# Kernel optimization log

Hardware: AMD Instinct MI355X
Metric: run time of the kernel (lower is better)

Reference implementation:

```python
import jax, jax.numpy as jnp
import numpy as np

B, SQ, SK, D = 8, 4096, 4096, 64


def setup_inputs() -> dict:
    key = jax.random.key(0)
    k1, k2, k3 = jax.random.split(key, 3)
    x1 = jax.random.normal(k1, (B, SQ, D), dtype=jnp.float32)   # queries
    x2 = jax.random.normal(k2, (B, SK, D), dtype=jnp.float32)   # keys
    x3 = jax.random.normal(k3, (B, SK, D), dtype=jnp.float32)   # values
    x4 = 0                                                      # dropout p (static, 0 => deterministic)
    x5 = jnp.ones((1,), dtype=jnp.float32)                      # scale divisor
    return {"x1": x1, "x2": x2, "x3": x3, "x4": x4, "x5": x5}


def reference(x1, x2, x3, x4, x5):
    # scores: [B, Sq, Sk]
    scores = jnp.einsum("bqd,bkd->bqk", x1, x2) / x5
    attn = jax.nn.softmax(scores, axis=-1)
    p = float(x4)  # static python scalar
    if p > 0.0:
        mask = jax.random.bernoulli(jax.random.key(42), 1.0 - p, attn.shape)
        attn = attn * mask.astype(attn.dtype) / (1.0 - p)
    # out: [B, Sq, D]
    return jnp.einsum("bqk,bkd->bqd", attn, x3)
```

## Files before the change

kernel.cpp:

```cpp
#include <hip/hip_runtime.h>


typedef _Float16 f16x8 __attribute__((ext_vector_type(8)));
typedef _Float16 f16x4 __attribute__((ext_vector_type(4)));
typedef __fp16   h16x2 __attribute__((ext_vector_type(2)));
typedef float    f32x4 __attribute__((ext_vector_type(4)));

constexpr int kB  = 8;
constexpr int kSQ = 4096;
constexpr int kSK = 4096;
constexpr int kD  = 64;
constexpr int KSPLIT = 4;
constexpr int SKH = kSK / KSPLIT;
constexpr int BQ  = 256;
constexpr int MT  = 4;
constexpr int BK  = 64;
constexpr size_t APART = (size_t)kB * kSQ * kD;
constexpr float kLog2e = 1.44269504088896340736f;

static __device__ __forceinline__ f16x4 pack4(float a, float b, float c, float d) {
    h16x2 p0 = __builtin_amdgcn_cvt_pkrtz(a, b);
    h16x2 p1 = __builtin_amdgcn_cvt_pkrtz(c, d);
    f16x4 r;
    r[0] = (_Float16)p0[0]; r[1] = (_Float16)p0[1];
    r[2] = (_Float16)p1[0]; r[3] = (_Float16)p1[1];
    return r;
}
static __device__ __forceinline__ f16x8 pack8(const float4& a, const float4& c) {
    f16x4 lo = pack4(a.x, a.y, a.z, a.w);
    f16x4 hi = pack4(c.x, c.y, c.z, c.w);
    f16x8 f;
    f[0] = lo[0]; f[1] = lo[1]; f[2] = lo[2]; f[3] = lo[3];
    f[4] = hi[0]; f[5] = hi[1]; f[6] = hi[2]; f[7] = hi[3];
    return f;
}

typedef const __attribute__((address_space(1))) unsigned int* gu32p;
typedef __attribute__((address_space(3))) unsigned int* lu32p;
static __device__ __forceinline__ void gload_lds16(const void* g, void* l) {
    __builtin_amdgcn_global_load_lds((gu32p)g, (lu32p)l, 16, 0, 0);
}

__global__ __launch_bounds__(256, 2)
void fattn_prepass(const float* __restrict__ Kg,
                   const float* __restrict__ Vg,
                   _Float16* __restrict__ Kh,
                   _Float16* __restrict__ Vt)
{
    __shared__ _Float16 tr[kD][BK];

    const int tid = threadIdx.x;
    const int kt  = blockIdx.x;
    const int b   = blockIdx.y;

    const int k = tid >> 2;
    const int p = tid & 3;
    const int gk = kt * BK + k;

    {
        const float* src = Kg + ((size_t)b * kSK + gk) * kD + p * 16;
        const float4 a0 = *(const float4*)(src + 0);
        const float4 a1 = *(const float4*)(src + 4);
        const float4 a2 = *(const float4*)(src + 8);
        const float4 a3 = *(const float4*)(src + 12);
        _Float16* dst = Kh + ((size_t)b * kSK + gk) * kD;
        const int fb0 = 2 * p, fb1 = 2 * p + 1;
        *(f16x8*)&dst[(fb0 ^ (gk & 7)) * 8] = pack8(a0, a1);
        *(f16x8*)&dst[(fb1 ^ (gk & 7)) * 8] = pack8(a2, a3);
    }
    {
        const float* src = Vg + ((size_t)b * kSK + gk) * kD + p * 16;
        const float4 a0 = *(const float4*)(src + 0);
        const float4 a1 = *(const float4*)(src + 4);
        const float4 a2 = *(const float4*)(src + 8);
        const float4 a3 = *(const float4*)(src + 12);
        const float v[16] = {a0.x,a0.y,a0.z,a0.w, a1.x,a1.y,a1.z,a1.w,
                             a2.x,a2.y,a2.z,a2.w, a3.x,a3.y,a3.z,a3.w};
#pragma unroll
        for (int j = 0; j < 16; ++j)
            tr[p * 16 + j][k] = (_Float16)v[j];
    }
    __syncthreads();
    {
        const int f  = tid >> 2;
        const int p2 = tid & 3;
        const f16x8 b0 = *(const f16x8*)&tr[f][p2 * 16 + 0];
        const f16x8 b1 = *(const f16x8*)&tr[f][p2 * 16 + 8];
        _Float16* dst = Vt + (((size_t)b * 64 + kt) * kD + f) * BK;
        const int kb0 = 2 * p2, kb1 = 2 * p2 + 1;
        *(f16x8*)&dst[(kb0 ^ (f & 7)) * 8] = b0;
        *(f16x8*)&dst[(kb1 ^ (f & 7)) * 8] = b1;
    }
}

__global__ __launch_bounds__(256, 2)
void fattn_partial(const float* __restrict__ Qg,
                   const _Float16* __restrict__ Kh,
                   const _Float16* __restrict__ Vt,
                   const float* __restrict__ sdiv,
                   _Float16* __restrict__ Ap,
                   float2* __restrict__ MLp)
{
    __shared__ __align__(16) _Float16 sK[2][BK * kD];
    __shared__ __align__(16) _Float16 sV[2][kD * BK];
    __shared__ __align__(16) _Float16 sP[4][16][BK];

    const int tid  = threadIdx.x;
    const int w    = tid >> 6;
    const int lane = tid & 63;
    const int l16  = lane & 15;
    const int quad = lane >> 4;
    const int sw   = (quad ^ (l16 & 7)) * 8;
    const int swp  = (l16 & 7) * 8;

    const int flat = blockIdx.x;
    const int c    = flat & 31;
    const int qi   = flat >> 5;
    const int b    = c >> 2;
    const int ks   = c & 3;
    const int qb   = qi * BQ;

    const float qscale = kLog2e / sdiv[0];

    const float* Qb = Qg + ((size_t)b * kSQ + qb) * kD;
    const _Float16* Khb = Kh + ((size_t)b * kSK + (size_t)ks * SKH) * kD;
    const _Float16* Vtb = Vt + (((size_t)b * 64 + (size_t)ks * (SKH / BK)) * kD) * BK;

    f16x8 qf[MT][2];
#pragma unroll
    for (int mt = 0; mt < MT; ++mt) {
        const float* qrow = Qb + (size_t)(w * 64 + mt * 16 + l16) * kD;
#pragma unroll
        for (int kk = 0; kk < 2; ++kk) {
            const float4 a = *(const float4*)(qrow + kk * 32 + quad * 8);
            const float4 cc = *(const float4*)(qrow + kk * 32 + quad * 8 + 4);
            float4 as = make_float4(a.x * qscale, a.y * qscale, a.z * qscale, a.w * qscale);
            float4 cs = make_float4(cc.x * qscale, cc.y * qscale, cc.z * qscale, cc.w * qscale);
            qf[mt][kk] = pack8(as, cs);
        }
    }

    f16x8 ones;
#pragma unroll
    for (int j = 0; j < 8; ++j) ones[j] = (_Float16)1.0f;

    auto stage = [&](int kt, int buf) {
        const char* gk = (const char*)(Khb + (size_t)kt * BK * kD) + w * 2048 + lane * 16;
        const char* gv = (const char*)(Vtb + (size_t)kt * kD * BK) + w * 2048 + lane * 16;
        char* lk = (char*)&sK[buf][0] + w * 2048;
        char* lv = (char*)&sV[buf][0] + w * 2048;
        gload_lds16(gk,        lk);
        gload_lds16(gk + 1024, lk + 1024);
        gload_lds16(gv,        lv);
        gload_lds16(gv + 1024, lv + 1024);
    };

    f32x4 o[MT][4];
    f32x4 ol[MT];
    float m_i[MT];
#pragma unroll
    for (int mt = 0; mt < MT; ++mt) {
        m_i[mt] = -1e30f;
#pragma unroll
        for (int r = 0; r < 4; ++r) ol[mt][r] = 0.0f;
#pragma unroll
        for (int dt = 0; dt < 4; ++dt)
#pragma unroll
            for (int r = 0; r < 4; ++r) o[mt][dt][r] = 0.0f;
    }

    stage(0, 0);
    __syncthreads();

    const int nIter = SKH / BK;
    for (int kt = 0; kt < nIter; ++kt) {
        const int buf = kt & 1;
        const bool more = (kt + 1 < nIter);
        if (more) stage(kt + 1, buf ^ 1);

        f32x4 s[MT][4];
#pragma unroll
        for (int nt = 0; nt < 4; ++nt) {
            const int krow = (nt * 16 + l16) * kD;
            const f16x8 kf0 = *(const f16x8*)&sK[buf][krow + sw];
            const f16x8 kf1 = *(const f16x8*)&sK[buf][krow + (sw ^ 32)];
#pragma unroll
            for (int mt = 0; mt < MT; ++mt) {
                f32x4 acc;
#pragma unroll
                for (int r = 0; r < 4; ++r) acc[r] = 0.0f;
                acc = __builtin_amdgcn_mfma_f32_16x16x32_f16(kf0, qf[mt][0], acc, 0, 0, 0);
                acc = __builtin_amdgcn_mfma_f32_16x16x32_f16(kf1, qf[mt][1], acc, 0, 0, 0);
                s[mt][nt] = acc;
            }
        }

        f16x8 vf[4][2];
#pragma unroll
        for (int dt = 0; dt < 4; ++dt) {
            const int frow = (dt * 16 + l16) * BK;
            vf[dt][0] = *(const f16x8*)&sV[buf][frow + sw];
            vf[dt][1] = *(const f16x8*)&sV[buf][frow + (sw ^ 32)];
        }

#pragma unroll
        for (int mt = 0; mt < MT; ++mt) {
            float ra = fmaxf(fmaxf(s[mt][0][0], s[mt][0][1]), fmaxf(s[mt][0][2], s[mt][0][3]));
            float rb = fmaxf(fmaxf(s[mt][1][0], s[mt][1][1]), fmaxf(s[mt][1][2], s[mt][1][3]));
            float rc = fmaxf(fmaxf(s[mt][2][0], s[mt][2][1]), fmaxf(s[mt][2][2], s[mt][2][3]));
            float rd = fmaxf(fmaxf(s[mt][3][0], s[mt][3][1]), fmaxf(s[mt][3][2], s[mt][3][3]));
            float rm = fmaxf(fmaxf(ra, rb), fmaxf(rc, rd));
            rm = fmaxf(rm, __shfl_xor(rm, 16, 64));
            rm = fmaxf(rm, __shfl_xor(rm, 32, 64));
            const float mnew = fmaxf(m_i[mt], rm);
#pragma unroll
            for (int nt = 0; nt < 4; ++nt)
#pragma unroll
                for (int r = 0; r < 4; ++r)
                    s[mt][nt][r] = __builtin_amdgcn_exp2f(s[mt][nt][r] - mnew);
            if (!__all(mnew == m_i[mt])) {
                const float alpha = __builtin_amdgcn_exp2f(m_i[mt] - mnew);
                ol[mt][0] *= alpha;
#pragma unroll
                for (int dt = 0; dt < 4; ++dt)
#pragma unroll
                    for (int r = 0; r < 4; ++r) o[mt][dt][r] *= alpha;
            }
            m_i[mt] = mnew;

#pragma unroll
            for (int nt = 0; nt < 4; ++nt)
                *(f16x4*)&sP[w][l16][(nt * 16 + quad * 4) ^ swp] =
                    pack4(s[mt][nt][0], s[mt][nt][1], s[mt][nt][2], s[mt][nt][3]);

            const f16x8 pf0 = *(const f16x8*)&sP[w][l16][(quad * 8) ^ swp];
            const f16x8 pf1 = *(const f16x8*)&sP[w][l16][(32 + quad * 8) ^ swp];
#pragma unroll
            for (int dt = 0; dt < 4; ++dt) {
                o[mt][dt] = __builtin_amdgcn_mfma_f32_16x16x32_f16(vf[dt][0], pf0, o[mt][dt], 0, 0, 0);
                o[mt][dt] = __builtin_amdgcn_mfma_f32_16x16x32_f16(vf[dt][1], pf1, o[mt][dt], 0, 0, 0);
            }
            ol[mt] = __builtin_amdgcn_mfma_f32_16x16x32_f16(ones, pf0, ol[mt], 0, 0, 0);
            ol[mt] = __builtin_amdgcn_mfma_f32_16x16x32_f16(ones, pf1, ol[mt], 0, 0, 0);
        }

        __syncthreads();
    }

    _Float16* Ab = Ap + (size_t)ks * APART + ((size_t)b * kSQ + qb) * kD;
    float2* MLb = MLp + (size_t)ks * kB * kSQ + (size_t)b * kSQ + qb;
#pragma unroll
    for (int mt = 0; mt < MT; ++mt) {
        const int row = w * 64 + mt * 16 + l16;
#pragma unroll
        for (int dt = 0; dt < 4; ++dt)
            *(f16x4*)&Ab[(size_t)row * kD + dt * 16 + quad * 4] =
                pack4(o[mt][dt][0], o[mt][dt][1], o[mt][dt][2], o[mt][dt][3]);
        if (quad == 0) MLb[row] = make_float2(m_i[mt], ol[mt][0]);
    }
}

__global__ __launch_bounds__(256)
void fattn_combine(const _Float16* __restrict__ Ap,
                   const float2* __restrict__ MLp,
                   float* __restrict__ Og)
{
    const int idx = blockIdx.x * 256 + threadIdx.x;
    const int r = idx >> 4;
    const int c = (idx & 15) * 4;

    float m = -1e30f;
    float2 ml[KSPLIT];
#pragma unroll
    for (int s = 0; s < KSPLIT; ++s) {
        ml[s] = MLp[(size_t)s * kB * kSQ + r];
        m = fmaxf(m, ml[s].x);
    }
    float acc[4] = {0.f, 0.f, 0.f, 0.f};
    float lsum = 0.f;
#pragma unroll
    for (int s = 0; s < KSPLIT; ++s) {
        const float e = __builtin_amdgcn_exp2f(ml[s].x - m);
        lsum += e * ml[s].y;
        const f16x4 a = *(const f16x4*)&Ap[(size_t)s * APART + (size_t)r * kD + c];
#pragma unroll
        for (int j = 0; j < 4; ++j) acc[j] += e * (float)a[j];
    }
    const float inv = 1.0f / lsum;
    float4 res = make_float4(acc[0] * inv, acc[1] * inv, acc[2] * inv, acc[3] * inv);
    *(float4*)&Og[(size_t)r * kD + c] = res;
}

extern "C" void kernel_launch(void* const* d_in, const int* in_sizes, int n_in,
                              void* d_out, int out_size, void* d_ws, size_t ws_size,
                              hipStream_t stream) {
    const float* Q    = (const float*)d_in[0];
    const float* K    = (const float*)d_in[1];
    const float* V    = (const float*)d_in[2];
    const float* sdiv = (const float*)d_in[4];
    float* O = (float*)d_out;

    _Float16* Kh  = (_Float16*)d_ws;
    _Float16* Vt  = Kh + (size_t)kB * kSK * kD;
    _Float16* Ap  = Vt + (size_t)kB * kSK * kD;
    float2*   MLp = (float2*)(Ap + (size_t)KSPLIT * APART);

    fattn_prepass<<<dim3(kSK / BK, kB), dim3(256), 0, stream>>>(K, V, Kh, Vt);
    fattn_partial<<<dim3((kSQ / BQ) * kB * KSPLIT), dim3(256), 0, stream>>>(Q, Kh, Vt, sdiv, Ap, MLp);
    fattn_combine<<<dim3(kB * kSQ * kD / (256 * 4)), dim3(256), 0, stream>>>(Ap, MLp, O);
}
```

Measured before the change: 138.8 us.

## Switch attention partial kernel to 32x32x16 MFMA with register-resident P via permlane swap

Rewrites the partial attention kernel to use 32x32x16 MFMA tiles with one 32-row query tile per wave and BQ reduced to 128. The P matrix is repacked in registers with permlane32_swap instead of going through LDS, and the row sum is accumulated with scalar adds instead of a ones-MFMA. Launch bounds are raised to allow 4 blocks per CU. The aim is to cut LDS traffic and per-tile MFMA overhead and to raise occupancy. In exchange, each block does less work on the K/V tiles it loads, so global and LDS staging per query grows.

```diff
diff --git a/kernel.cpp b/kernel.cpp
--- a/kernel.cpp
+++ b/kernel.cpp
@@ -5,6 +5,7 @@
 typedef _Float16 f16x4 __attribute__((ext_vector_type(4)));
 typedef __fp16   h16x2 __attribute__((ext_vector_type(2)));
 typedef float    f32x4 __attribute__((ext_vector_type(4)));
+typedef float    f32x16 __attribute__((ext_vector_type(16)));
 
 constexpr int kB  = 8;
 constexpr int kSQ = 4096;
@@ -12,8 +13,7 @@
 constexpr int kD  = 64;
 constexpr int KSPLIT = 4;
 constexpr int SKH = kSK / KSPLIT;
-constexpr int BQ  = 256;
-constexpr int MT  = 4;
+constexpr int BQ  = 128;
 constexpr int BK  = 64;
 constexpr size_t APART = (size_t)kB * kSQ * kD;
 constexpr float kLog2e = 1.44269504088896340736f;
@@ -34,12 +34,29 @@
     f[4] = hi[0]; f[5] = hi[1]; f[6] = hi[2]; f[7] = hi[3];
     return f;
 }
+static __device__ __forceinline__ unsigned pkrtz_u(float a, float b) {
+    union { h16x2 h; unsigned u; } cv;
+    cv.h = __builtin_amdgcn_cvt_pkrtz(a, b);
+    return cv.u;
+}
 
 typedef const __attribute__((address_space(1))) unsigned int* gu32p;
 typedef __attribute__((address_space(3))) unsigned int* lu32p;
 static __device__ __forceinline__ void gload_lds16(const void* g, void* l) {
     __builtin_amdgcn_global_load_lds((gu32p)g, (lu32p)l, 16, 0, 0);
 }
+
+#define PA_SLICE(dst, sv, rb) do {                                          \
+    unsigned c0 = pkrtz_u((sv)[(rb)+0], (sv)[(rb)+1]);                      \
+    unsigned c1 = pkrtz_u((sv)[(rb)+2], (sv)[(rb)+3]);                      \
+    unsigned c2 = pkrtz_u((sv)[(rb)+4], (sv)[(rb)+5]);                      \
+    unsigned c3 = pkrtz_u((sv)[(rb)+6], (sv)[(rb)+7]);                      \
+    auto r02 = __builtin_amdgcn_permlane32_swap(c0, c2, false, false);      \
+    auto r13 = __builtin_amdgcn_permlane32_swap(c1, c3, false, false);      \
+    union { unsigned u[4]; f16x8 v; } _r;                                   \
+    _r.u[0] = r02[0]; _r.u[1] = r13[0]; _r.u[2] = r02[1]; _r.u[3] = r13[1]; \
+    dst = _r.v;                                                             \
+} while (0)
 
 __global__ __launch_bounds__(256, 2)
 void fattn_prepass(const float* __restrict__ Kg,
@@ -93,7 +110,7 @@
     }
 }
 
-__global__ __launch_bounds__(256, 2)
+__global__ __launch_bounds__(256, 4)
 void fattn_partial(const float* __restrict__ Qg,
                    const _Float16* __restrict__ Kh,
                    const _Float16* __restrict__ Vt,
@@ -103,15 +120,12 @@
 {
     __shared__ __align__(16) _Float16 sK[2][BK * kD];
     __shared__ __align__(16) _Float16 sV[2][kD * BK];
-    __shared__ __align__(16) _Float16 sP[4][16][BK];
 
     const int tid  = threadIdx.x;
     const int w    = tid >> 6;
     const int lane = tid & 63;
-    const int l16  = lane & 15;
-    const int quad = lane >> 4;
-    const int sw   = (quad ^ (l16 & 7)) * 8;
-    const int swp  = (l16 & 7) * 8;
+    const int l31  = lane & 31;
+    const int hi   = lane >> 5;
 
     const int flat = blockIdx.x;
     const int c    = flat & 31;
@@ -126,23 +140,23 @@
     const _Float16* Khb = Kh + ((size_t)b * kSK + (size_t)ks * SKH) * kD;
     const _Float16* Vtb = Vt + (((size_t)b * 64 + (size_t)ks * (SKH / BK)) * kD) * BK;
 
-    f16x8 qf[MT][2];
-#pragma unroll
-    for (int mt = 0; mt < MT; ++mt) {
-        const float* qrow = Qb + (size_t)(w * 64 + mt * 16 + l16) * kD;
-#pragma unroll
-        for (int kk = 0; kk < 2; ++kk) {
-            const float4 a = *(const float4*)(qrow + kk * 32 + quad * 8);
-            const float4 cc = *(const float4*)(qrow + kk * 32 + quad * 8 + 4);
+    f16x8 qf[4];
+    {
+        const float* qrow = Qb + (size_t)(w * 32 + l31) * kD;
+#pragma unroll
+        for (int ds = 0; ds < 4; ++ds) {
+            const float4 a  = *(const float4*)(qrow + ds * 16 + hi * 8);
+            const float4 cc = *(const float4*)(qrow + ds * 16 + hi * 8 + 4);
             float4 as = make_float4(a.x * qscale, a.y * qscale, a.z * qscale, a.w * qscale);
             float4 cs = make_float4(cc.x * qscale, cc.y * qscale, cc.z * qscale, cc.w * qscale);
-            qf[mt][kk] = pack8(as, cs);
-        }
-    }
-
-    f16x8 ones;
-#pragma unroll
-    for (int j = 0; j < 8; ++j) ones[j] = (_Float16)1.0f;
+            qf[ds] = pack8(as, cs);
+        }
+    }
+
+    int offA[4];
+#pragma unroll
+    for (int i = 0; i < 4; ++i)
+        offA[i] = l31 * 64 + (((2 * i + hi) ^ (l31 & 7)) * 8);
 
     auto stage = [&](int kt, int buf) {
         const char* gk = (const char*)(Khb + (size_t)kt * BK * kD) + w * 2048 + lane * 16;
@@ -155,19 +169,11 @@
         gload_lds16(gv + 1024, lv + 1024);
     };
 
-    f32x4 o[MT][4];
-    f32x4 ol[MT];
-    float m_i[MT];
-#pragma unroll
-    for (int mt = 0; mt < MT; ++mt) {
-        m_i[mt] = -1e30f;
-#pragma unroll
-        for (int r = 0; r < 4; ++r) ol[mt][r] = 0.0f;
-#pragma unroll
-        for (int dt = 0; dt < 4; ++dt)
-#pragma unroll
-            for (int r = 0; r < 4; ++r) o[mt][dt][r] = 0.0f;
-    }
+    f32x16 o0, o1;
+#pragma unroll
+    for (int r = 0; r < 16; ++r) { o0[r] = 0.0f; o1[r] = 0.0f; }
+    float m_i = -1e30f;
+    float ll  = 0.0f;
 
     stage(0, 0);
     __syncthreads();
@@ -175,73 +181,70 @@
     const int nIter = SKH / BK;
     for (int kt = 0; kt < nIter; ++kt) {
         const int buf = kt & 1;
-        const bool more = (kt + 1 < nIter);
-        if (more) stage(kt + 1, buf ^ 1);
-
-        f32x4 s[MT][4];
-#pragma unroll
-        for (int nt = 0; nt < 4; ++nt) {
-            const int krow = (nt * 16 + l16) * kD;
-            const f16x8 kf0 = *(const f16x8*)&sK[buf][krow + sw];
-            const f16x8 kf1 = *(const f16x8*)&sK[buf][krow + (sw ^ 32)];
-#pragma unroll
-            for (int mt = 0; mt < MT; ++mt) {
-                f32x4 acc;
-#pragma unroll
-                for (int r = 0; r < 4; ++r) acc[r] = 0.0f;
-                acc = __builtin_amdgcn_mfma_f32_16x16x32_f16(kf0, qf[mt][0], acc, 0, 0, 0);
-                acc = __builtin_amdgcn_mfma_f32_16x16x32_f16(kf1, qf[mt][1], acc, 0, 0, 0);
-                s[mt][nt] = acc;
+        if (kt + 1 < nIter) stage(kt + 1, buf ^ 1);
+
+        f32x16 s0, s1;
+#pragma unroll
+        for (int r = 0; r < 16; ++r) { s0[r] = 0.0f; s1[r] = 0.0f; }
+#pragma unroll
+        for (int ds = 0; ds < 4; ++ds) {
+            const f16x8 kf0 = *(const f16x8*)&sK[buf][offA[ds]];
+            const f16x8 kf1 = *(const f16x8*)&sK[buf][offA[ds] + 2048];
+            s0 = __builtin_amdgcn_mfma_f32_32x32x16_f16(kf0, qf[ds], s0, 0, 0, 0);
+            s1 = __builtin_amdgcn_mfma_f32_32x32x16_f16(kf1, qf[ds], s1, 0, 0, 0);
+        }
+
+        f16x8 vf[4][2];
+#pragma unroll
+        for (int s = 0; s < 4; ++s) {
+            vf[s][0] = *(const f16x8*)&sV[buf][offA[s]];
+            vf[s][1] = *(const f16x8*)&sV[buf][offA[s] + 2048];
+        }
+
+        float t[16];
+#pragma unroll
+        for (int r = 0; r < 16; ++r) t[r] = fmaxf(s0[r], s1[r]);
+#pragma unroll
+        for (int r = 0; r < 8; ++r)  t[r] = fmaxf(t[r], t[r + 8]);
+#pragma unroll
+        for (int r = 0; r < 4; ++r)  t[r] = fmaxf(t[r], t[r + 4]);
+        float rm = fmaxf(fmaxf(t[0], t[1]), fmaxf(t[2], t[3]));
+        rm = fmaxf(rm, __shfl_xor(rm, 32, 64));
+        const float mnew = fmaxf(m_i, rm);
+
+#pragma unroll
+        for (int r = 0; r < 16; ++r) {
+            s0[r] = __builtin_amdgcn_exp2f(s0[r] - mnew);
+            s1[r] = __builtin_amdgcn_exp2f(s1[r] - mnew);
+        }
+        if (!__all(mnew == m_i)) {
+            const float alpha = __builtin_amdgcn_exp2f(m_i - mnew);
+            ll *= alpha;
+#pragma unroll
+            for (int r = 0; r < 16; ++r) { o0[r] *= alpha; o1[r] *= alpha; }
+        }
+        m_i = mnew;
+
+        {
+            float a0 = 0.f, a1 = 0.f, a2 = 0.f, a3 = 0.f;
+#pragma unroll
+            for (int r = 0; r < 16; r += 4) {
+                a0 += s0[r]; a1 += s0[r + 1]; a2 += s0[r + 2]; a3 += s0[r + 3];
+                a0 += s1[r]; a1 += s1[r + 1]; a2 += s1[r + 2]; a3 += s1[r + 3];
             }
-        }
-
-        f16x8 vf[4][2];
-#pragma unroll
-        for (int dt = 0; dt < 4; ++dt) {
-            const int frow = (dt * 16 + l16) * BK;
-            vf[dt][0] = *(const f16x8*)&sV[buf][frow + sw];
-            vf[dt][1] = *(const f16x8*)&sV[buf][frow + (sw ^ 32)];
-        }
-
-#pragma unroll
-        for (int mt = 0; mt < MT; ++mt) {
-            float ra = fmaxf(fmaxf(s[mt][0][0], s[mt][0][1]), fmaxf(s[mt][0][2], s[mt][0][3]));
-            float rb = fmaxf(fmaxf(s[mt][1][0], s[mt][1][1]), fmaxf(s[mt][1][2], s[mt][1][3]));
-            float rc = fmaxf(fmaxf(s[mt][2][0], s[mt][2][1]), fmaxf(s[mt][2][2], s[mt][2][3]));
-            float rd = fmaxf(fmaxf(s[mt][3][0], s[mt][3][1]), fmaxf(s[mt][3][2], s[mt][3][3]));
-            float rm = fmaxf(fmaxf(ra, rb), fmaxf(rc, rd));
-            rm = fmaxf(rm, __shfl_xor(rm, 16, 64));
-            rm = fmaxf(rm, __shfl_xor(rm, 32, 64));
-            const float mnew = fmaxf(m_i[mt], rm);
-#pragma unroll
-            for (int nt = 0; nt < 4; ++nt)
-#pragma unroll
-                for (int r = 0; r < 4; ++r)
-                    s[mt][nt][r] = __builtin_amdgcn_exp2f(s[mt][nt][r] - mnew);
-            if (!__all(mnew == m_i[mt])) {
-                const float alpha = __builtin_amdgcn_exp2f(m_i[mt] - mnew);
-                ol[mt][0] *= alpha;
-#pragma unroll
-                for (int dt = 0; dt < 4; ++dt)
-#pragma unroll
-                    for (int r = 0; r < 4; ++r) o[mt][dt][r] *= alpha;
-            }
-            m_i[mt] = mnew;
-
-#pragma unroll
-            for (int nt = 0; nt < 4; ++nt)
-                *(f16x4*)&sP[w][l16][(nt * 16 + quad * 4) ^ swp] =
-                    pack4(s[mt][nt][0], s[mt][nt][1], s[mt][nt][2], s[mt][nt][3]);
-
-            const f16x8 pf0 = *(const f16x8*)&sP[w][l16][(quad * 8) ^ swp];
-            const f16x8 pf1 = *(const f16x8*)&sP[w][l16][(32 + quad * 8) ^ swp];
-#pragma unroll
-            for (int dt = 0; dt < 4; ++dt) {
-                o[mt][dt] = __builtin_amdgcn_mfma_f32_16x16x32_f16(vf[dt][0], pf0, o[mt][dt], 0, 0, 0);
-                o[mt][dt] = __builtin_amdgcn_mfma_f32_16x16x32_f16(vf[dt][1], pf1, o[mt][dt], 0, 0, 0);
-            }
-            ol[mt] = __builtin_amdgcn_mfma_f32_16x16x32_f16(ones, pf0, ol[mt], 0, 0, 0);
-            ol[mt] = __builtin_amdgcn_mfma_f32_16x16x32_f16(ones, pf1, ol[mt], 0, 0, 0);
+            ll += (a0 + a1) + (a2 + a3);
+        }
+
+        f16x8 pa[4];
+        PA_SLICE(pa[0], s0, 0);
+        PA_SLICE(pa[1], s0, 8);
+        PA_SLICE(pa[2], s1, 0);
+        PA_SLICE(pa[3], s1, 8);
+
+#pragma unroll
+        for (int s = 0; s < 4; ++s) {
+            o0 = __builtin_amdgcn_mfma_f32_32x32x16_f16(vf[s][0], pa[s], o0, 0, 0, 0);
+            o1 = __builtin_amdgcn_mfma_f32_32x32x16_f16(vf[s][1], pa[s], o1, 0, 0, 0);
         }
 
         __syncthreads();
@@ -249,14 +252,18 @@
 
     _Float16* Ab = Ap + (size_t)ks * APART + ((size_t)b * kSQ + qb) * kD;
     float2* MLb = MLp + (size_t)ks * kB * kSQ + (size_t)b * kSQ + qb;
-#pragma unroll
-    for (int mt = 0; mt < MT; ++mt) {
-        const int row = w * 64 + mt * 16 + l16;
-#pragma unroll
-        for (int dt = 0; dt < 4; ++dt)
-            *(f16x4*)&Ab[(size_t)row * kD + dt * 16 + quad * 4] =
-                pack4(o[mt][dt][0], o[mt][dt][1], o[mt][dt][2], o[mt][dt][3]);
-        if (quad == 0) MLb[row] = make_float2(m_i[mt], ol[mt][0]);
+    const int q = w * 32 + l31;
+    _Float16* arow = &Ab[(size_t)q * kD];
+#pragma unroll
+    for (int g = 0; g < 4; ++g) {
+        *(f16x4*)&arow[g * 8 + hi * 4] =
+            pack4(o0[4 * g], o0[4 * g + 1], o0[4 * g + 2], o0[4 * g + 3]);
+        *(f16x4*)&arow[32 + g * 8 + hi * 4] =
+            pack4(o1[4 * g], o1[4 * g + 1], o1[4 * g + 2], o1[4 * g + 3]);
+    }
+    {
+        const float lf = ll + __shfl_xor(ll, 32, 64);
+        if (hi == 0) MLb[q] = make_float2(m_i, lf);
     }
 }
 
```

Result: slower. 143.0 us (+3.0%).
